# Kernel optimization log

Measured on AMD Instinct MI355X. Metric: run time of the kernel, lower is better.

Reference implementation:

```python
import jax, jax.numpy as jnp
import numpy as np

N, D, S = 16384, 8, 8192
DIAG_FILL = 5.0


def setup_inputs() -> dict:
    key = jax.random.key(0)
    k1, k2, k3 = jax.random.split(key, 3)
    latent_z = jax.random.normal(k1, (N, D), dtype=jnp.float32)
    # relation entries kept away from 0 since they appear in a denominator
    relation = jax.random.uniform(k2, (N, N), dtype=jnp.float32) + 0.5
    sample_idx = jax.random.randint(k3, (S,), 0, N)
    return {"latent_z": latent_z, "relation": relation, "sample_idx": sample_idx}


def _safe_sqrt(x):
    # sqrt with zero gradient at 0 (matches torch.cdist subgradient on the diagonal)
    pos = x > 0
    return jnp.where(pos, jnp.sqrt(jnp.where(pos, x, 1.0)), 0.0)


def reference(latent_z, relation, sample_idx):
    z = latent_z[sample_idx]                      # [S, D]
    rel = relation[sample_idx][:, sample_idx]     # [S, S]
    sq = jnp.sum(z * z, axis=-1)                  # [S]
    d2 = jnp.maximum(sq[:, None] + sq[None, :] - 2.0 * (z @ z.T), 0.0)
    dist = _safe_sqrt(d2)                         # torch.cdist(z, z), p=2
    # denominator is a fresh copy of rel with diagonal filled to 5 (fill_diagonal_
    # mutates only the second advanced-indexing copy in the torch code)
    ii = jnp.arange(z.shape[0])
    den = rel.at[ii, ii].set(DIAG_FILL)
    return jnp.sqrt(jnp.sum((dist - rel) ** 2 / den))
```

## Files before the change

### kernel.cpp

```cpp
#include <hip/hip_runtime.h>
#include <math.h>

#define NFULL 16384
#define SN 8192
#define DIM 8
#define DIAG_FILL 5.0f

#define OFF_ACC   0
#define OFF_HIST  256
#define OFF_OFFS  (OFF_HIST + NFULL * 4)
#define OFF_CSORT (OFF_OFFS + NFULL * 4)
#define OFF_SQG   (OFF_CSORT + SN * 4)
#define OFF_ZG    (OFF_SQG + SN * 4)

__global__ void hist_kernel(const int* __restrict__ sample_idx, int* __restrict__ hist) {
    int t = blockIdx.x * 256 + threadIdx.x;
    atomicAdd(&hist[sample_idx[t]], 1);
}

__global__ void scan_kernel(const int* __restrict__ hist, int* __restrict__ offs) {
    __shared__ int tot[1024];
    int t = threadIdx.x;
    int base = t * 16;
    int loc[16];
    int s = 0;
    #pragma unroll
    for (int k = 0; k < 16; k++) { loc[k] = s; s += hist[base + k]; }
    int val = s;
    tot[t] = val;
    __syncthreads();
    for (int off = 1; off < 1024; off <<= 1) {
        int add = (t >= off) ? tot[t - off] : 0;
        __syncthreads();
        val += add;
        tot[t] = val;
        __syncthreads();
    }
    int excl = val - s;
    #pragma unroll
    for (int k = 0; k < 16; k++) offs[base + k] = excl + loc[k];
}

__global__ void scatter_kernel(const int* __restrict__ hist, const int* __restrict__ offs,
                               int* __restrict__ csort) {
    int b = blockIdx.x * 256 + threadIdx.x;
    int st = offs[b], cnt = hist[b];
    for (int k = 0; k < cnt; k++) csort[st + k] = b;
}

__global__ void gatherz_kernel(const float* __restrict__ latent_z, const int* __restrict__ csort,
                               float* __restrict__ zg, float* __restrict__ sqg) {
    int a = blockIdx.x * 256 + threadIdx.x;
    int r = csort[a];
    const float4* src = (const float4*)(latent_z + (size_t)r * DIM);
    float4 u = src[0], v = src[1];
    float4* dst = (float4*)(zg + (size_t)a * DIM);
    dst[0] = u; dst[1] = v;
    sqg[a] = u.x*u.x + u.y*u.y + u.z*u.z + u.w*u.w
           + v.x*v.x + v.y*v.y + v.z*v.z + v.w*v.w;
}

__global__ __launch_bounds__(256) void
main_kernel(const float* __restrict__ relation, const int* __restrict__ csort,
            const float* __restrict__ zg, const float* __restrict__ sqg,
            float* __restrict__ acc) {
    int jg = blockIdx.x & 31;
    int ic = blockIdx.x >> 5;
    int t = threadIdx.x;
    int j = jg * 256 + t;

    int cj = csort[j];
    const float4* zj4 = (const float4*)(zg + (size_t)j * DIM);
    float4 p = zj4[0], q = zj4[1];
    float sqj = sqg[j];

    float sum = 0.f;
    int a0 = ic * 128;
    #pragma unroll 4
    for (int k = 0; k < 128; k++) {
        int a = a0 + k;
        int r = csort[a];
        const float4* za4 = (const float4*)(zg + (size_t)a * DIM);
        float4 u = za4[0], v = za4[1];
        float sqa = sqg[a];
        float rel = relation[((size_t)r << 14) + cj];
        float dot = u.x*p.x + u.y*p.y + u.z*p.z + u.w*p.w
                  + v.x*q.x + v.y*q.y + v.z*q.z + v.w*q.w;
        float d2 = fmaxf(sqa + sqj - 2.f * dot, 0.f);
        float dist = sqrtf(d2);
        float den = rel;
        if (a == j) { dist = 0.f; den = DIAG_FILL; }
        float d = dist - rel;
        sum += d * d * __builtin_amdgcn_rcpf(den);
    }

    #pragma unroll
    for (int o = 32; o > 0; o >>= 1) sum += __shfl_down(sum, o, 64);
    __shared__ float part[4];
    int lane = t & 63, w = t >> 6;
    if (lane == 0) part[w] = sum;
    __syncthreads();
    if (t == 0) atomicAdd(acc, part[0] + part[1] + part[2] + part[3]);
}

__global__ void final_kernel(const float* __restrict__ acc, float* __restrict__ out) {
    out[0] = sqrtf(acc[0]);
}

extern "C" void kernel_launch(void* const* d_in, const int* in_sizes, int n_in,
                              void* d_out, int out_size, void* d_ws, size_t ws_size,
                              hipStream_t stream) {
    const float* latent_z  = (const float*)d_in[0];
    const float* relation  = (const float*)d_in[1];
    const int*   sample_idx = (const int*)d_in[2];
    float* out = (float*)d_out;

    char* ws = (char*)d_ws;
    float* acc  = (float*)(ws + OFF_ACC);
    int*  hist  = (int*)(ws + OFF_HIST);
    int*  offs  = (int*)(ws + OFF_OFFS);
    int*  csort = (int*)(ws + OFF_CSORT);
    float* sqg  = (float*)(ws + OFF_SQG);
    float* zg   = (float*)(ws + OFF_ZG);

    hipMemsetAsync(d_ws, 0, OFF_HIST + NFULL * 4, stream);

    hist_kernel<<<SN / 256, 256, 0, stream>>>(sample_idx, hist);
    scan_kernel<<<1, 1024, 0, stream>>>(hist, offs);
    scatter_kernel<<<NFULL / 256, 256, 0, stream>>>(hist, offs, csort);
    gatherz_kernel<<<SN / 256, 256, 0, stream>>>(latent_z, csort, zg, sqg);
    main_kernel<<<2048, 256, 0, stream>>>(relation, csort, zg, sqg, acc);
    final_kernel<<<1, 1, 0, stream>>>(acc, out);
}
```

Baseline: 1.231 ms.

## Fuse preprocessing into one block kernel and stage sample tile in LDS

Merges the histogram, scan, scatter and z-gather launches into a single 1024-thread prep kernel, using shared memory for the sorted index list and zeroing the accumulator there. The main kernel now loads each block's 128 sampled rows (z, squared norm, row offset) into shared memory once instead of having every thread reread them from global memory on each iteration, and unrolls the loop further. This cuts launch overhead and redundant global loads. The cost is serialising the prep work onto a single block.

```diff
diff --git a/kernel.cpp b/kernel.cpp
--- a/kernel.cpp
+++ b/kernel.cpp
@@ -8,62 +8,70 @@
 
 #define OFF_ACC   0
 #define OFF_HIST  256
-#define OFF_OFFS  (OFF_HIST + NFULL * 4)
-#define OFF_CSORT (OFF_OFFS + NFULL * 4)
+#define OFF_CSORT (OFF_HIST + NFULL * 4)
 #define OFF_SQG   (OFF_CSORT + SN * 4)
 #define OFF_ZG    (OFF_SQG + SN * 4)
 
-__global__ void hist_kernel(const int* __restrict__ sample_idx, int* __restrict__ hist) {
-    int t = blockIdx.x * 256 + threadIdx.x;
-    atomicAdd(&hist[sample_idx[t]], 1);
-}
+__global__ __launch_bounds__(1024) void prep_kernel(
+    const float* __restrict__ latent_z, const int* __restrict__ sample_idx,
+    int* __restrict__ hist, int* __restrict__ csort,
+    float* __restrict__ zg, float* __restrict__ sqg, float* __restrict__ acc) {
+    __shared__ int partial[1024];
+    __shared__ int csl[SN];
+    int t = threadIdx.x;
 
-__global__ void scan_kernel(const int* __restrict__ hist, int* __restrict__ offs) {
-    __shared__ int tot[1024];
-    int t = threadIdx.x;
+    #pragma unroll
+    for (int k = 0; k < 8; k++) atomicAdd(&hist[sample_idx[k * 1024 + t]], 1);
+    __syncthreads();
+
     int base = t * 16;
-    int loc[16];
-    int s = 0;
+    int cnt[16], loc[16], s = 0;
     #pragma unroll
-    for (int k = 0; k < 16; k++) { loc[k] = s; s += hist[base + k]; }
+    for (int k = 0; k < 16; k++) {
+        cnt[k] = __hip_atomic_load(&hist[base + k], __ATOMIC_RELAXED, __HIP_MEMORY_SCOPE_AGENT);
+        loc[k] = s; s += cnt[k];
+    }
     int val = s;
-    tot[t] = val;
+    partial[t] = val;
     __syncthreads();
     for (int off = 1; off < 1024; off <<= 1) {
-        int add = (t >= off) ? tot[t - off] : 0;
+        int add = (t >= off) ? partial[t - off] : 0;
         __syncthreads();
         val += add;
-        tot[t] = val;
+        partial[t] = val;
         __syncthreads();
     }
     int excl = val - s;
+
     #pragma unroll
-    for (int k = 0; k < 16; k++) offs[base + k] = excl + loc[k];
-}
+    for (int k = 0; k < 16; k++) {
+        int st = excl + loc[k];
+        for (int c = 0; c < cnt[k]; c++) { csl[st + c] = base + k; csort[st + c] = base + k; }
+    }
+    __syncthreads();
 
-__global__ void scatter_kernel(const int* __restrict__ hist, const int* __restrict__ offs,
-                               int* __restrict__ csort) {
-    int b = blockIdx.x * 256 + threadIdx.x;
-    int st = offs[b], cnt = hist[b];
-    for (int k = 0; k < cnt; k++) csort[st + k] = b;
-}
-
-__global__ void gatherz_kernel(const float* __restrict__ latent_z, const int* __restrict__ csort,
-                               float* __restrict__ zg, float* __restrict__ sqg) {
-    int a = blockIdx.x * 256 + threadIdx.x;
-    int r = csort[a];
-    const float4* src = (const float4*)(latent_z + (size_t)r * DIM);
-    float4 u = src[0], v = src[1];
-    float4* dst = (float4*)(zg + (size_t)a * DIM);
-    dst[0] = u; dst[1] = v;
-    sqg[a] = u.x*u.x + u.y*u.y + u.z*u.z + u.w*u.w
-           + v.x*v.x + v.y*v.y + v.z*v.z + v.w*v.w;
+    #pragma unroll
+    for (int k = 0; k < 8; k++) {
+        int a = k * 1024 + t;
+        int r = csl[a];
+        const float4* src = (const float4*)(latent_z + (size_t)r * DIM);
+        float4 u = src[0], v = src[1];
+        float4* dst = (float4*)(zg + (size_t)a * DIM);
+        dst[0] = u; dst[1] = v;
+        sqg[a] = u.x*u.x + u.y*u.y + u.z*u.z + u.w*u.w
+               + v.x*v.x + v.y*v.y + v.z*v.z + v.w*v.w;
+    }
+    if (t == 0) acc[0] = 0.f;
 }
 
 __global__ __launch_bounds__(256) void
 main_kernel(const float* __restrict__ relation, const int* __restrict__ csort,
             const float* __restrict__ zg, const float* __restrict__ sqg,
             float* __restrict__ acc) {
+    __shared__ float zs[128 * 8];
+    __shared__ float sqs[128];
+    __shared__ int   ro[128];
+
     int jg = blockIdx.x & 31;
     int ic = blockIdx.x >> 5;
     int t = threadIdx.x;
@@ -74,22 +82,31 @@
     float4 p = zj4[0], q = zj4[1];
     float sqj = sqg[j];
 
+    if (t < 128) {
+        int a = ic * 128 + t;
+        int r = csort[a];
+        ro[t] = r << 14;
+        const float4* za4 = (const float4*)(zg + (size_t)a * DIM);
+        ((float4*)(zs + t * 8))[0] = za4[0];
+        ((float4*)(zs + t * 8))[1] = za4[1];
+        sqs[t] = sqg[a];
+    }
+    __syncthreads();
+
+    int kd = j - ic * 128;
     float sum = 0.f;
-    int a0 = ic * 128;
-    #pragma unroll 4
+    #pragma unroll 8
     for (int k = 0; k < 128; k++) {
-        int a = a0 + k;
-        int r = csort[a];
-        const float4* za4 = (const float4*)(zg + (size_t)a * DIM);
-        float4 u = za4[0], v = za4[1];
-        float sqa = sqg[a];
-        float rel = relation[((size_t)r << 14) + cj];
+        float rel = relation[(size_t)(unsigned)(ro[k] + cj)];
+        const float4* zk = (const float4*)(zs + k * 8);
+        float4 u = zk[0], v = zk[1];
+        float sqa = sqs[k];
         float dot = u.x*p.x + u.y*p.y + u.z*p.z + u.w*p.w
                   + v.x*q.x + v.y*q.y + v.z*q.z + v.w*q.w;
         float d2 = fmaxf(sqa + sqj - 2.f * dot, 0.f);
         float dist = sqrtf(d2);
         float den = rel;
-        if (a == j) { dist = 0.f; den = DIAG_FILL; }
+        if (k == kd) { dist = 0.f; den = DIAG_FILL; }
         float d = dist - rel;
         sum += d * d * __builtin_amdgcn_rcpf(den);
     }
@@ -110,25 +127,21 @@
 extern "C" void kernel_launch(void* const* d_in, const int* in_sizes, int n_in,
                               void* d_out, int out_size, void* d_ws, size_t ws_size,
                               hipStream_t stream) {
-    const float* latent_z  = (const float*)d_in[0];
-    const float* relation  = (const float*)d_in[1];
+    const float* latent_z   = (const float*)d_in[0];
+    const float* relation   = (const float*)d_in[1];
     const int*   sample_idx = (const int*)d_in[2];
     float* out = (float*)d_out;
 
     char* ws = (char*)d_ws;
     float* acc  = (float*)(ws + OFF_ACC);
     int*  hist  = (int*)(ws + OFF_HIST);
-    int*  offs  = (int*)(ws + OFF_OFFS);
     int*  csort = (int*)(ws + OFF_CSORT);
     float* sqg  = (float*)(ws + OFF_SQG);
     float* zg   = (float*)(ws + OFF_ZG);
 
     hipMemsetAsync(d_ws, 0, OFF_HIST + NFULL * 4, stream);
 
-    hist_kernel<<<SN / 256, 256, 0, stream>>>(sample_idx, hist);
-    scan_kernel<<<1, 1024, 0, stream>>>(hist, offs);
-    scatter_kernel<<<NFULL / 256, 256, 0, stream>>>(hist, offs, csort);
-    gatherz_kernel<<<SN / 256, 256, 0, stream>>>(latent_z, csort, zg, sqg);
+    prep_kernel<<<1, 1024, 0, stream>>>(latent_z, sample_idx, hist, csort, zg, sqg, acc);
     main_kernel<<<2048, 256, 0, stream>>>(relation, csort, zg, sqg, acc);
     final_kernel<<<1, 1, 0, stream>>>(acc, out);
 }
```

New measurement: 1.262 ms. 1.02x slower.
